# Optimization experiments

Hardware: AMD Instinct MI355X
Metric: run time of the kernel (lower is better)

## Reference

```python
import jax, jax.numpy as jnp
import numpy as np
import math

DIM = 4096
N_HEADS = 32
N_KV_HEADS = 8
HEAD_DIM = DIM // N_HEADS          # 128
N_REP = N_HEADS // N_KV_HEADS      # 4
BATCH = 2
SEQ = 2048
ROPE_THETA = 10000.0


def rope_cos_sin(seq_len, head_dim, theta=ROPE_THETA):
    # matches precompute_freqs_cis: freqs over even indices, outer with positions
    inv_freq = 1.0 / (theta ** (jnp.arange(0, head_dim, 2, dtype=jnp.float32) / head_dim))
    t = jnp.arange(seq_len, dtype=jnp.float32)
    ang = jnp.outer(t, inv_freq)          # [S, head_dim//2]
    return jnp.cos(ang), jnp.sin(ang)


def apply_rope(x, cos, sin):
    # x: [B, S, H, D]; consecutive pairs (x0, x1) form complex numbers (view_as_complex)
    x0 = x[..., 0::2]
    x1 = x[..., 1::2]
    c = cos[None, :, None, :]
    s = sin[None, :, None, :]
    r0 = x0 * c - x1 * s
    r1 = x0 * s + x1 * c
    return jnp.stack([r0, r1], axis=-1).reshape(x.shape)


def setup_inputs() -> dict:
    key = jax.random.key(0)
    ks = jax.random.split(key, 5)
    scale = 1.0 / math.sqrt(DIM)
    return {
        "x": jax.random.normal(ks[0], (BATCH, SEQ, DIM), dtype=jnp.float32),
        "wq": jax.random.normal(ks[1], (DIM, N_HEADS * HEAD_DIM), dtype=jnp.float32) * scale,
        "wk": jax.random.normal(ks[2], (DIM, N_KV_HEADS * HEAD_DIM), dtype=jnp.float32) * scale,
        "wv": jax.random.normal(ks[3], (DIM, N_KV_HEADS * HEAD_DIM), dtype=jnp.float32) * scale,
        "wo": jax.random.normal(ks[4], (N_HEADS * HEAD_DIM, DIM), dtype=jnp.float32) * scale,
        "start_pos": 0,
    }


def reference(x, wq, wk, wv, wo, start_pos):
    B, S, _ = x.shape
    # projections
    q = (x @ wq).reshape(B, S, N_HEADS, HEAD_DIM)
    k = (x @ wk).reshape(B, S, N_KV_HEADS, HEAD_DIM)
    v = (x @ wv).reshape(B, S, N_KV_HEADS, HEAD_DIM)
    # RoPE on q, k (training path: full-sequence freqs)
    cos, sin = rope_cos_sin(S, HEAD_DIM)
    q = apply_rope(q, cos, sin)
    k = apply_rope(k, cos, sin)
    # GQA: repeat_kv expands kv heads by n_rep
    k = jnp.repeat(k, N_REP, axis=2)  # [B, S, H, D]
    v = jnp.repeat(v, N_REP, axis=2)
    # [B, H, S, D]
    q = q.transpose(0, 2, 1, 3)
    k = k.transpose(0, 2, 1, 3)
    v = v.transpose(0, 2, 1, 3)
    scores = jnp.einsum("bhqd,bhkd->bhqk", q, k) / math.sqrt(HEAD_DIM)
    # causal mask: -inf above diagonal
    mask = jnp.triu(jnp.full((S, S), float("-inf"), dtype=scores.dtype), k=1)
    scores = scores + mask[None, None]
    attn = jax.nn.softmax(scores.astype(jnp.float32), axis=-1).astype(q.dtype)
    out = jnp.einsum("bhqk,bhkd->bhqd", attn, v)
    out = out.transpose(0, 2, 1, 3).reshape(B, S, N_HEADS * HEAD_DIM)
    return out @ wo
```

## Files before the change

### kernel.cpp

```cpp
#include <hip/hip_runtime.h>

#define DIM 4096
#define HD 128
#define NH 32
#define NKV 8
#define SEQ 2048
#define BATCH 2
#define MTOT (BATCH*SEQ)
#define GK DIM

typedef __bf16 bf16;
typedef __bf16 bf16x4 __attribute__((ext_vector_type(4)));
typedef __bf16 bf16x8 __attribute__((ext_vector_type(8)));
typedef float f32x4 __attribute__((ext_vector_type(4)));

__device__ __forceinline__ void gload_lds16(const void* g, void* l) {
    __builtin_amdgcn_global_load_lds(
        (const __attribute__((address_space(1))) void*)g,
        (__attribute__((address_space(3))) void*)l, 16, 0, 0);
}

__global__ __launch_bounds__(256) void conv_bf16(const float* __restrict__ in,
                                                 bf16* __restrict__ out, int n8) {
    int i = blockIdx.x * 256 + threadIdx.x;
    if (i >= n8) return;
    const float4* p = (const float4*)(in + (size_t)i * 8);
    float4 a = p[0], b = p[1];
    bf16x8 v;
    v[0]=(bf16)a.x; v[1]=(bf16)a.y; v[2]=(bf16)a.z; v[3]=(bf16)a.w;
    v[4]=(bf16)b.x; v[5]=(bf16)b.y; v[6]=(bf16)b.z; v[7]=(bf16)b.w;
    *(bf16x8*)(out + (size_t)i * 8) = v;
}

__global__ __launch_bounds__(256) void tconv(const float* __restrict__ in,
                                             bf16* __restrict__ out, int N, int K) {
    __shared__ float t[32][33];
    int bx = blockIdx.x, by = blockIdx.y;
    int tx = threadIdx.x, ty = threadIdx.y;
    int col = bx * 32 + tx;
#pragma unroll
    for (int r = 0; r < 4; ++r) {
        int row = by * 32 + ty + r * 8;
        t[ty + r * 8][tx] = in[(size_t)row * N + col];
    }
    __syncthreads();
#pragma unroll
    for (int r = 0; r < 4; ++r) {
        int n = bx * 32 + ty + r * 8;
        int k = by * 32 + tx;
        out[(size_t)n * K + k] = (bf16)t[tx][ty + r * 8];
    }
}

__global__ __launch_bounds__(256) void rope_k(bf16* __restrict__ buf, int shift, int n8) {
    int i = blockIdx.x * 256 + threadIdx.x;
    if (i >= n8) return;
    size_t base = (size_t)i * 8;
    int col = (int)(base & ((1u << shift) - 1));
    int pos = (int)((base >> shift) & (SEQ - 1));
    int d0 = col & (HD - 1);
    bf16x8 v = *(const bf16x8*)(buf + base);
    float f[8];
#pragma unroll
    for (int j = 0; j < 8; ++j) f[j] = (float)v[j];
    const float nl2t = -13.287712379549449f / 64.f;
#pragma unroll
    for (int j = 0; j < 4; ++j) {
        float inv = exp2f(nl2t * (float)((d0 >> 1) + j));
        float ang = (float)pos * inv;
        float sn, cs;
        sincosf(ang, &sn, &cs);
        float x0 = f[2 * j], x1 = f[2 * j + 1];
        f[2 * j]     = x0 * cs - x1 * sn;
        f[2 * j + 1] = x0 * sn + x1 * cs;
    }
    bf16x8 ov;
#pragma unroll
    for (int j = 0; j < 8; ++j) ov[j] = (bf16)f[j];
    *(bf16x8*)(buf + base) = ov;
}

template <bool F32OUT>
__global__ __launch_bounds__(256) void gemm_bt(const bf16* __restrict__ A,
                                               const bf16* __restrict__ Bt,
                                               void* __restrict__ out0, int N) {
    __shared__ alignas(16) bf16 sA[2][128 * 32];
    __shared__ alignas(16) bf16 sB[2][128 * 32];
    const int tid = threadIdx.x;
    const int lane = tid & 63, wid = tid >> 6;
    const int wm = wid >> 1, wn = wid & 1;
    const int m0 = blockIdx.y * 128, n0 = blockIdx.x * 128;

    auto stage = [&](int buf, int kt) {
#pragma unroll
        for (int it = 0; it < 2; ++it) {
            int slot = it * 256 + tid;
            int row = slot >> 2, s = slot & 3;
            gload_lds16(A + (size_t)(m0 + row) * GK + kt * 32 + s * 8, &sA[buf][slot * 8]);
            gload_lds16(Bt + (size_t)(n0 + row) * GK + kt * 32 + s * 8, &sB[buf][slot * 8]);
        }
    };

    f32x4 acc[4][4] = {};
    stage(0, 0);
    __syncthreads();
    int cur = 0;
    for (int kt = 0; kt < GK / 32; ++kt) {
        if (kt + 1 < GK / 32) stage(cur ^ 1, kt + 1);
        bf16x8 bF[4], aF[4];
#pragma unroll
        for (int i = 0; i < 4; ++i)
            bF[i] = *(const bf16x8*)&sB[cur][(wn * 64 + i * 16 + (lane & 15)) * 32 + (lane >> 4) * 8];
#pragma unroll
        for (int i = 0; i < 4; ++i)
            aF[i] = *(const bf16x8*)&sA[cur][(wm * 64 + i * 16 + (lane & 15)) * 32 + (lane >> 4) * 8];
#pragma unroll
        for (int mi = 0; mi < 4; ++mi)
#pragma unroll
            for (int ni = 0; ni < 4; ++ni)
                acc[mi][ni] = __builtin_amdgcn_mfma_f32_16x16x32_bf16(aF[mi], bF[ni], acc[mi][ni], 0, 0, 0);
        __syncthreads();
        cur ^= 1;
    }
#pragma unroll
    for (int mi = 0; mi < 4; ++mi) {
#pragma unroll
        for (int ni = 0; ni < 4; ++ni) {
#pragma unroll
            for (int r = 0; r < 4; ++r) {
                int row = m0 + wm * 64 + mi * 16 + (lane >> 4) * 4 + r;
                int col = n0 + wn * 64 + ni * 16 + (lane & 15);
                float v = acc[mi][ni][r];
                if constexpr (F32OUT) {
                    ((float*)out0)[(size_t)row * N + col] = v;
                } else {
                    ((bf16*)out0)[(size_t)row * N + col] = (bf16)v;
                }
            }
        }
    }
}

template <bool F32OUT>
__global__ __launch_bounds__(512, 2) void gemm8(const bf16* __restrict__ A,
                                                const bf16* __restrict__ Bt,
                                                void* __restrict__ outp, int N) {
    __shared__ alignas(16) char sA[2][2][16384];
    __shared__ alignas(16) char sB[2][2][16384];
    const int tid = threadIdx.x, lane = tid & 63;
    const int wid = tid >> 6;
    const int wm = wid >> 2, wn = wid & 3;
    const int m0 = blockIdx.y * 256, n0 = blockIdx.x * 256;
    const int lrow = lane & 15, hc = lane >> 4;
    const int rowbase = ((lrow >> 1) * 128) +
                        (((((lrow & 1) << 2) | hc) ^ (lrow >> 1)) << 4);
    const int NT = GK / 64;

    auto stageR = [&](int t, int kh) {
#pragma unroll
        for (int it = 0; it < 2; ++it) {
            int sl = it * 512 + tid;
            int PRr = sl >> 3, ps = sl & 7;
            int lsl = ps ^ (PRr & 7);
            int r = PRr * 2 + (lsl >> 2);
            int cc = lsl & 3;
            size_t koff = (size_t)t * 64 + kh * 32 + cc * 8;
            gload_lds16(A + (size_t)(m0 + r) * GK + koff, &sA[t & 1][kh][sl * 16]);
            gload_lds16(Bt + (size_t)(n0 + r) * GK + koff, &sB[t & 1][kh][sl * 16]);
        }
    };

    f32x4 acc[8][4] = {};

    stageR(0, 0); stageR(0, 1);
    asm volatile("s_waitcnt vmcnt(4)" ::: "memory");
    __builtin_amdgcn_s_barrier();

    for (int t = 0; t < NT; ++t) {
#pragma unroll
        for (int kh = 0; kh < 2; ++kh) {
            const char* Ab = &sA[t & 1][kh][0];
            const char* Bb = &sB[t & 1][kh][0];
            bf16x8 bf[4], af[8];
#pragma unroll
            for (int ni = 0; ni < 4; ++ni)
                bf[ni] = *(const bf16x8*)(Bb + wn * 4096 + ni * 1024 + rowbase);
#pragma unroll
            for (int mi = 0; mi < 8; ++mi)
                af[mi] = *(const bf16x8*)(Ab + wm * 8192 + mi * 1024 + rowbase);
            if (t + 1 < NT) {
                stageR(t + 1, kh);
                asm volatile("s_waitcnt vmcnt(4)" ::: "memory");
            } else {
                asm volatile("s_waitcnt vmcnt(0)" ::: "memory");
            }
            __builtin_amdgcn_s_barrier();
            __builtin_amdgcn_sched_barrier(0);
            __builtin_amdgcn_s_setprio(1);
#pragma unroll
            for (int mi = 0; mi < 8; ++mi)
#pragma unroll
                for (int ni = 0; ni < 4; ++ni)
                    acc[mi][ni] = __builtin_amdgcn_mfma_f32_16x16x32_bf16(af[mi], bf[ni], acc[mi][ni], 0, 0, 0);
            __builtin_amdgcn_s_setprio(0);
        }
    }

#pragma unroll
    for (int mi = 0; mi < 8; ++mi)
#pragma unroll
        for (int ni = 0; ni < 4; ++ni)
#pragma unroll
            for (int r = 0; r < 4; ++r) {
                int row = m0 + wm * 128 + mi * 16 + hc * 4 + r;
                int col = n0 + wn * 64 + ni * 16 + lrow;
                if constexpr (F32OUT)
                    ((float*)outp)[(size_t)row * N + col] = acc[mi][ni][r];
                else
                    ((bf16*)outp)[(size_t)row * N + col] = (bf16)acc[mi][ni][r];
            }
}

__global__ __launch_bounds__(512, 4) void attn_fwd(const bf16* __restrict__ q,
                                                   const bf16* __restrict__ k,
                                                   const bf16* __restrict__ vt,
                                                   bf16* __restrict__ o) {
    __shared__ alignas(16) bf16 sK[2][64 * 128];
    __shared__ alignas(16) bf16 sV[2][128 * 64];
    __shared__ alignas(16) bf16 sP[8][16 * 64];
    const int tid = threadIdx.x, lane = tid & 63, wid = tid >> 6;
    const int bi = blockIdx.x;
    const int pr = bi & 7;
    const int h = (bi >> 3) & 31;
    const int b = bi >> 8;
    const int kvh = h >> 2;
    const float scale = 0.08838834764831845f;

    const bf16* kb0 = k + (size_t)b * SEQ * (NKV * HD) + kvh * HD;
    const bf16* vb0 = vt + (size_t)(kvh * HD) * MTOT + (size_t)b * SEQ;

    auto stage = [&](int bf, int tt) {
#pragma unroll
        for (int it = 0; it < 2; ++it) {
            int slot = it * 512 + tid;
            int row = slot >> 4, s = slot & 15;
            gload_lds16(kb0 + (size_t)(tt * 64 + row) * (NKV * HD) + ((s ^ (row & 7)) * 8),
                        &sK[bf][slot * 8]);
        }
#pragma unroll
        for (int it = 0; it < 2; ++it) {
            int slot = it * 512 + tid;
            int row = slot >> 3, s = slot & 7;
            gload_lds16(vb0 + (size_t)row * MTOT + tt * 64 + ((s ^ (row & 7)) * 8),
                        &sV[bf][slot * 8]);
        }
    };

    auto pass = [&](int qt) {
        const int qb0 = qt * 128;
        const int nt = 2 * qt + 2;
        const bf16* qp = q + ((size_t)(b * SEQ + qb0 + wid * 16 + (lane & 15))) * DIM
                           + h * HD + (lane >> 4) * 8;
        bf16x8 aQ[4];
#pragma unroll
        for (int ks = 0; ks < 4; ++ks) aQ[ks] = *(const bf16x8*)(qp + ks * 32);

        f32x4 accO[8] = {};
        float m_r = -1e30f, l_r = 0.f;
        const int qglob = qb0 + wid * 16 + (lane & 15);
        char* pb = (char*)&sP[wid][0];
        const int q7s = (lane & 7) << 4;
        const int hi = lane >> 4;

        stage(0, 0);
        __syncthreads();
        int cur = 0;
        for (int tt = 0; tt < nt; ++tt) {
            if (tt + 1 < nt) stage(cur ^ 1, tt + 1);
            if (tt * 64 <= qb0 + wid * 16 + 15) {
                f32x4 accS[4] = {};
#pragma unroll
                for (int nt2 = 0; nt2 < 4; ++nt2) {
                    int kr = nt2 * 16 + (lane & 15);
#pragma unroll
                    for (int ks = 0; ks < 4; ++ks) {
                        int slog = ks * 4 + hi;
                        bf16x8 bK = *(const bf16x8*)&sK[cur][kr * 128 + ((slog ^ (kr & 7)) * 8)];
                        accS[nt2] = __builtin_amdgcn_mfma_f32_16x16x32_bf16(bK, aQ[ks], accS[nt2], 0, 0, 0);
                    }
                }

                const bool diag = (tt * 64 + 63 > qb0 + wid * 16);
                const int kvb = tt * 64 + hi * 4;
                float mx = -1e30f;
#pragma unroll
                for (int nt2 = 0; nt2 < 4; ++nt2)
#pragma unroll
                    for (int r = 0; r < 4; ++r) {
                        float v = accS[nt2][r] * scale;
                        if (diag && (kvb + nt2 * 16 + r > qglob)) v = -1e30f;
                        accS[nt2][r] = v;
                        mx = fmaxf(mx, v);
                    }
                mx = fmaxf(mx, __shfl_xor(mx, 16, 64));
                mx = fmaxf(mx, __shfl_xor(mx, 32, 64));

                float mn = fmaxf(m_r, mx);
                float al = __expf(m_r - mn);
                m_r = mn;
                float rs = 0.f;
#pragma unroll
                for (int nt2 = 0; nt2 < 4; ++nt2)
#pragma unroll
                    for (int r = 0; r < 4; ++r) {
                        float p = __expf(accS[nt2][r] - mn);
                        accS[nt2][r] = p;
                        rs += p;
                    }
                rs += __shfl_xor(rs, 16, 64);
                rs += __shfl_xor(rs, 32, 64);
                l_r = l_r * al + rs;

                float al4[4];
#pragma unroll
                for (int r = 0; r < 4; ++r) al4[r] = __shfl(al, hi * 4 + r, 64);
#pragma unroll
                for (int d2 = 0; d2 < 8; ++d2)
#pragma unroll
                    for (int r = 0; r < 4; ++r) accO[d2][r] *= al4[r];

#pragma unroll
                for (int nt2 = 0; nt2 < 4; ++nt2) {
                    bf16x4 pv;
                    pv[0] = (bf16)accS[nt2][0]; pv[1] = (bf16)accS[nt2][1];
                    pv[2] = (bf16)accS[nt2][2]; pv[3] = (bf16)accS[nt2][3];
                    *(bf16x4*)(pb + (lane & 15) * 128 + ((nt2 * 32 + hi * 8) ^ q7s)) = pv;
                }

                bf16x8 aP[2];
#pragma unroll
                for (int kk = 0; kk < 2; ++kk)
                    aP[kk] = *(const bf16x8*)(pb + (lane & 15) * 128 + ((kk * 64 + hi * 16) ^ q7s));
#pragma unroll
                for (int d2 = 0; d2 < 8; ++d2) {
#pragma unroll
                    for (int kk = 0; kk < 2; ++kk) {
                        int dv = d2 * 16 + (lane & 15);
                        int phys = (kk * 4 + hi) ^ (dv & 7);
                        bf16x8 bV = *(const bf16x8*)&sV[cur][dv * 64 + phys * 8];
                        accO[d2] = __builtin_amdgcn_mfma_f32_16x16x32_bf16(aP[kk], bV, accO[d2], 0, 0, 0);
                    }
                }
            }
            __syncthreads();
            cur ^= 1;
        }

        float linv[4];
#pragma unroll
        for (int r = 0; r < 4; ++r) linv[r] = 1.f / __shfl(l_r, hi * 4 + r, 64);
        size_t orow = (size_t)(b * SEQ + qb0 + wid * 16 + hi * 4) * DIM
                    + h * HD + (lane & 15);
#pragma unroll
        for (int d2 = 0; d2 < 8; ++d2)
#pragma unroll
            for (int r = 0; r < 4; ++r)
                o[orow + (size_t)r * DIM + d2 * 16] = (bf16)(accO[d2][r] * linv[r]);
    };

    pass(pr);
    pass(15 - pr);
}

extern "C" void kernel_launch(void* const* d_in, const int* in_sizes, int n_in,
                              void* d_out, int out_size, void* d_ws, size_t ws_size,
                              hipStream_t stream) {
    const float* x  = (const float*)d_in[0];
    const float* wq = (const float*)d_in[1];
    const float* wk = (const float*)d_in[2];
    const float* wv = (const float*)d_in[3];
    const float* wo = (const float*)d_in[4];
    float* out = (float*)d_out;

    char* ws = (char*)d_ws;
    size_t off = 0;
    bf16* xb  = (bf16*)(ws + off); off += (size_t)MTOT * DIM * 2;
    bf16* wqt = (bf16*)(ws + off); off += (size_t)DIM * DIM * 2;
    bf16* wkt = (bf16*)(ws + off); off += (size_t)1024 * DIM * 2;
    bf16* wvt = (bf16*)(ws + off); off += (size_t)1024 * DIM * 2;
    bf16* qb  = (bf16*)(ws + off); off += (size_t)MTOT * DIM * 2;
    bf16* kb  = (bf16*)(ws + off); off += (size_t)MTOT * 1024 * 2;
    bf16* vtb = (bf16*)(ws + off); off += (size_t)MTOT * 1024 * 2;
    bf16* ao = xb;

    dim3 tb(32, 8);
    conv_bf16<<<(MTOT * DIM / 8) / 256, 256, 0, stream>>>(x, xb, MTOT * DIM / 8);
    tconv<<<dim3(DIM / 32, DIM / 32), tb, 0, stream>>>(wq, wqt, DIM, DIM);
    tconv<<<dim3(1024 / 32, DIM / 32), tb, 0, stream>>>(wk, wkt, 1024, DIM);
    tconv<<<dim3(1024 / 32, DIM / 32), tb, 0, stream>>>(wv, wvt, 1024, DIM);

    gemm8<false><<<dim3(DIM / 256, MTOT / 256), 512, 0, stream>>>(xb, wqt, qb, DIM);
    gemm_bt<false><<<dim3(1024 / 128, MTOT / 128), 256, 0, stream>>>(xb, wkt, kb, 1024);
    gemm_bt<false><<<dim3(MTOT / 128, 1024 / 128), 256, 0, stream>>>(wvt, xb, vtb, MTOT);

    rope_k<<<(MTOT * DIM / 8) / 256, 256, 0, stream>>>(qb, 12, MTOT * DIM / 8);
    rope_k<<<(MTOT * 1024 / 8) / 256, 256, 0, stream>>>(kb, 10, MTOT * 1024 / 8);

    tconv<<<dim3(DIM / 32, DIM / 32), tb, 0, stream>>>(wo, wqt, DIM, DIM);

    attn_fwd<<<BATCH * NH * 8, 512, 0, stream>>>(qb, kb, vtb, ao);

    gemm8<true><<<dim3(DIM / 256, MTOT / 256), 512, 0, stream>>>(ao, wqt, out, DIM);
}
```

Measured before the change: 627.6 us.

## Fold softmax scale and log2e into Q rope, add lazy rescaling in attention

Folds the 1/sqrt(d) softmax scale and log2(e) into the RoPE pass over Q so attention can use raw exp2 without a per-score multiply. Masking is restricted to diagonal tiles. The running-max rescale of the output accumulator is skipped when no row's max grows by more than 8 (log2 units), and the tile-skip condition is tightened to the warp's first query row. The goal is fewer VALU ops in the softmax inner loop. The trade-off is an extra rounding of scaled Q in bf16, and unnormalized exponents can reach up to 2^8, which fp32 handles.

```diff
diff --git a/kernel.cpp b/kernel.cpp
--- a/kernel.cpp
+++ b/kernel.cpp
@@ -52,7 +52,8 @@
     }
 }
 
-__global__ __launch_bounds__(256) void rope_k(bf16* __restrict__ buf, int shift, int n8) {
+__global__ __launch_bounds__(256) void rope_k(bf16* __restrict__ buf, int shift,
+                                              int n8, float oscale) {
     int i = blockIdx.x * 256 + threadIdx.x;
     if (i >= n8) return;
     size_t base = (size_t)i * 8;
@@ -76,7 +77,7 @@
     }
     bf16x8 ov;
 #pragma unroll
-    for (int j = 0; j < 8; ++j) ov[j] = (bf16)f[j];
+    for (int j = 0; j < 8; ++j) ov[j] = (bf16)(f[j] * oscale);
     *(bf16x8*)(buf + base) = ov;
 }
 
@@ -234,7 +235,6 @@
     const int h = (bi >> 3) & 31;
     const int b = bi >> 8;
     const int kvh = h >> 2;
-    const float scale = 0.08838834764831845f;
 
     const bf16* kb0 = k + (size_t)b * SEQ * (NKV * HD) + kvh * HD;
     const bf16* vb0 = vt + (size_t)(kvh * HD) * MTOT + (size_t)b * SEQ;
@@ -259,7 +259,8 @@
     auto pass = [&](int qt) {
         const int qb0 = qt * 128;
         const int nt = 2 * qt + 2;
-        const bf16* qp = q + ((size_t)(b * SEQ + qb0 + wid * 16 + (lane & 15))) * DIM
+        const int qw = qb0 + wid * 16;
+        const bf16* qp = q + ((size_t)(b * SEQ + qw + (lane & 15))) * DIM
                            + h * HD + (lane >> 4) * 8;
         bf16x8 aQ[4];
 #pragma unroll
@@ -267,7 +268,7 @@
 
         f32x4 accO[8] = {};
         float m_r = -1e30f, l_r = 0.f;
-        const int qglob = qb0 + wid * 16 + (lane & 15);
+        const int qglob = qw + (lane & 15);
         char* pb = (char*)&sP[wid][0];
         const int q7s = (lane & 7) << 4;
         const int hi = lane >> 4;
@@ -277,7 +278,7 @@
         int cur = 0;
         for (int tt = 0; tt < nt; ++tt) {
             if (tt + 1 < nt) stage(cur ^ 1, tt + 1);
-            if (tt * 64 <= qb0 + wid * 16 + 15) {
+            if (tt * 64 <= qw) {
                 f32x4 accS[4] = {};
 #pragma unroll
                 for (int nt2 = 0; nt2 < 4; ++nt2) {
@@ -290,44 +291,54 @@
                     }
                 }
 
-                const bool diag = (tt * 64 + 63 > qb0 + wid * 16);
-                const int kvb = tt * 64 + hi * 4;
+                const bool diag = (tt * 64 + 63 > qw);
                 float mx = -1e30f;
-#pragma unroll
-                for (int nt2 = 0; nt2 < 4; ++nt2)
-#pragma unroll
-                    for (int r = 0; r < 4; ++r) {
-                        float v = accS[nt2][r] * scale;
-                        if (diag && (kvb + nt2 * 16 + r > qglob)) v = -1e30f;
-                        accS[nt2][r] = v;
-                        mx = fmaxf(mx, v);
-                    }
+                if (diag) {
+                    const int kvb = tt * 64 + hi * 4;
+#pragma unroll
+                    for (int nt2 = 0; nt2 < 4; ++nt2)
+#pragma unroll
+                        for (int r = 0; r < 4; ++r) {
+                            float v = accS[nt2][r];
+                            if (kvb + nt2 * 16 + r > qglob) v = -1e30f;
+                            accS[nt2][r] = v;
+                            mx = fmaxf(mx, v);
+                        }
+                } else {
+#pragma unroll
+                    for (int nt2 = 0; nt2 < 4; ++nt2)
+#pragma unroll
+                        for (int r = 0; r < 4; ++r) mx = fmaxf(mx, accS[nt2][r]);
+                }
                 mx = fmaxf(mx, __shfl_xor(mx, 16, 64));
                 mx = fmaxf(mx, __shfl_xor(mx, 32, 64));
 
-                float mn = fmaxf(m_r, mx);
-                float al = __expf(m_r - mn);
-                m_r = mn;
+                if (!__all(mx <= m_r + 8.f)) {
+                    float mn = fmaxf(m_r, mx);
+                    float al = __builtin_amdgcn_exp2f(m_r - mn);
+                    m_r = mn;
+                    l_r *= al;
+                    float al4[4];
+#pragma unroll
+                    for (int r = 0; r < 4; ++r) al4[r] = __shfl(al, hi * 4 + r, 64);
+#pragma unroll
+                    for (int d2 = 0; d2 < 8; ++d2)
+#pragma unroll
+                        for (int r = 0; r < 4; ++r) accO[d2][r] *= al4[r];
+                }
+
                 float rs = 0.f;
 #pragma unroll
                 for (int nt2 = 0; nt2 < 4; ++nt2)
 #pragma unroll
                     for (int r = 0; r < 4; ++r) {
-                        float p = __expf(accS[nt2][r] - mn);
+                        float p = __builtin_amdgcn_exp2f(accS[nt2][r] - m_r);
                         accS[nt2][r] = p;
                         rs += p;
                     }
                 rs += __shfl_xor(rs, 16, 64);
                 rs += __shfl_xor(rs, 32, 64);
-                l_r = l_r * al + rs;
-
-                float al4[4];
-#pragma unroll
-                for (int r = 0; r < 4; ++r) al4[r] = __shfl(al, hi * 4 + r, 64);
-#pragma unroll
-                for (int d2 = 0; d2 < 8; ++d2)
-#pragma unroll
-                    for (int r = 0; r < 4; ++r) accO[d2][r] *= al4[r];
+                l_r += rs;
 
 #pragma unroll
                 for (int nt2 = 0; nt2 < 4; ++nt2) {
@@ -393,6 +404,8 @@
     bf16* vtb = (bf16*)(ws + off); off += (size_t)MTOT * 1024 * 2;
     bf16* ao = xb;
 
+    const float SCALE2 = 0.08838834764831845f * 1.44269504088896340f;
+
     dim3 tb(32, 8);
     conv_bf16<<<(MTOT * DIM / 8) / 256, 256, 0, stream>>>(x, xb, MTOT * DIM / 8);
     tconv<<<dim3(DIM / 32, DIM / 32), tb, 0, stream>>>(wq, wqt, DIM, DIM);
@@ -403,8 +416,8 @@
     gemm_bt<false><<<dim3(1024 / 128, MTOT / 128), 256, 0, stream>>>(xb, wkt, kb, 1024);
     gemm_bt<false><<<dim3(MTOT / 128, 1024 / 128), 256, 0, stream>>>(wvt, xb, vtb, MTOT);
 
-    rope_k<<<(MTOT * DIM / 8) / 256, 256, 0, stream>>>(qb, 12, MTOT * DIM / 8);
-    rope_k<<<(MTOT * 1024 / 8) / 256, 256, 0, stream>>>(kb, 10, MTOT * 1024 / 8);
+    rope_k<<<(MTOT * DIM / 8) / 256, 256, 0, stream>>>(qb, 12, MTOT * DIM / 8, SCALE2);
+    rope_k<<<(MTOT * 1024 / 8) / 256, 256, 0, stream>>>(kb, 10, MTOT * 1024 / 8, 1.0f);
 
     tconv<<<dim3(DIM / 32, DIM / 32), tb, 0, stream>>>(wo, wqt, DIM, DIM);
 
```

Result: faster. 609.0 us (-3.0%).
